# Kernel tuning notes

Measured on AMD Instinct MI355X. Metric: run time of the kernel, lower is better.

The kernel has to match this reference:

```python
import jax, jax.numpy as jnp
import numpy as np

BETA = 0.25
N_E = 1024
E_DIM = 64
B, L = 32, 2048


def setup_inputs() -> dict:
    key = jax.random.key(0)
    k1, k2 = jax.random.split(key)
    z = jax.random.normal(k1, (B, L, E_DIM), dtype=jnp.float32)
    # torch init: uniform_(-1/n_e, 1/n_e)
    codebook = jax.random.uniform(k2, (N_E, E_DIM), dtype=jnp.float32,
                                  minval=-1.0 / N_E, maxval=1.0 / N_E)
    return {"z": z, "codebook": codebook}


def reference(z, codebook):
    sg = jax.lax.stop_gradient
    n_e = codebook.shape[0]
    zf = z.reshape(-1, codebook.shape[1])  # (N, e_dim)
    # squared-distance matrix: ||z||^2 + ||e||^2 - 2 z.e  -> (N, n_e)
    d = (jnp.sum(zf * zf, axis=1, keepdims=True)
         + jnp.sum(codebook * codebook, axis=1)
         - 2.0 * zf @ codebook.T)
    idx = jnp.argmin(d, axis=1)  # (N,)
    # one-hot @ codebook is just a gather
    z_q = codebook[idx].reshape(z.shape)
    loss = (jnp.mean((sg(z_q) - z) ** 2)
            + BETA * jnp.mean((z_q - sg(z)) ** 2))
    # straight-through estimator
    z_q_st = z + sg(z_q - z)
    # codebook usage stats (mean of one-hot rows == normalized histogram)
    counts = jnp.zeros((n_e,), dtype=z.dtype).at[idx].add(1.0)
    e_mean = counts / idx.shape[0]
    perplexity = jnp.exp(-jnp.sum(e_mean * jnp.log(e_mean + 1e-10)))
    return loss, z_q_st, perplexity, idx
```

## Files before the change

### kernel.cpp

```cpp
#include <hip/hip_runtime.h>
#include <math.h>

#define E_DIM 64
#define N_E   1024
#define BETA  0.25
#define NROWS 65536

using bf16x8 = __attribute__((ext_vector_type(8))) short;
using f32x4  = __attribute__((ext_vector_type(4))) float;
#define MFMA(a, b, c) __builtin_amdgcn_mfma_f32_16x16x32_bf16((a), (b), (c), 0, 0, 0)


__device__ __forceinline__ unsigned short f2bf_rn(float f) {
    unsigned u = __builtin_bit_cast(unsigned, f);
    unsigned r = u + 0x7fffu + ((u >> 16) & 1u);
    return (unsigned short)(r >> 16);
}
__device__ __forceinline__ float bf2f(unsigned short b) {
    unsigned u = ((unsigned)b) << 16;
    return __builtin_bit_cast(float, u);
}

__device__ __forceinline__ float pw64_sq(const float* v) {
    float r[8];
#pragma unroll
    for (int l = 0; l < 8; ++l) r[l] = v[l] * v[l];
#pragma unroll
    for (int t = 1; t < 8; ++t)
#pragma unroll
        for (int l = 0; l < 8; ++l) r[l] += v[8 * t + l] * v[8 * t + l];
    return ((r[0] + r[1]) + (r[2] + r[3])) + ((r[4] + r[5]) + (r[6] + r[7]));
}

__global__ __launch_bounds__(256) void k_prep(const float* __restrict__ cb,
                                              unsigned short* __restrict__ ebh,
                                              unsigned short* __restrict__ ebl,
                                              float* __restrict__ h,
                                              unsigned* __restrict__ hist,
                                              double* __restrict__ sse,
                                              unsigned* __restrict__ flagN) {
    int t = blockIdx.x * 256 + threadIdx.x;
    {
        int e = t & 7, lane = (t >> 3) & 63, ks = (t >> 9) & 1, ct = t >> 10;
        int j = ct * 16 + (lane & 15);
        int k = ks * 32 + ((lane >> 4) << 3) + e;
        float v = cb[j * 64 + k];
        unsigned short hi = f2bf_rn(v);
        ebh[t] = hi;
        ebl[t] = f2bf_rn(v - bf2f(hi));
    }
    if (blockIdx.x < 4) {
        int j = t;
        float e[E_DIM];
        const float4* ep = reinterpret_cast<const float4*>(cb + (size_t)j * E_DIM);
#pragma unroll
        for (int k4 = 0; k4 < E_DIM / 4; ++k4) {
            float4 v = ep[k4];
            e[4 * k4 + 0] = v.x; e[4 * k4 + 1] = v.y;
            e[4 * k4 + 2] = v.z; e[4 * k4 + 3] = v.w;
        }
        h[j] = pw64_sq(e);
    } else if (blockIdx.x == 4) {
#pragma unroll
        for (int u = 0; u < 4; ++u) hist[threadIdx.x * 4 + u] = 0u;
    } else if (blockIdx.x == 5 && threadIdx.x == 0) {
        *sse = 0.0;
        *flagN = 0u;
    }
}

__global__ __launch_bounds__(512, 4) void k_mfma(
    const float* __restrict__ z, const float* __restrict__ cb,
    const float* __restrict__ h,
    const unsigned short* __restrict__ ebh, const unsigned short* __restrict__ ebl,
    float* __restrict__ out_zq, float* __restrict__ out_idx,
    unsigned* __restrict__ hist, double* __restrict__ sse,
    unsigned* __restrict__ flagN, unsigned* __restrict__ flagL) {
    const int lane = threadIdx.x & 63;
    const int w = __builtin_amdgcn_readfirstlane(threadIdx.x >> 6);
    const int m = lane & 15, g = lane >> 4;
    const int half = w >> 2;
    const int rw   = w & 3;

    __shared__ int bok;
    __shared__ float sh_h[N_E];
    __shared__ float rsv[128];
    __shared__ float sb0[2][128], sb1[2][128];
    __shared__ int   sbi[2][128];
    __shared__ float wp[8];
    if (threadIdx.x == 0) bok = 1;
    for (int i = threadIdx.x; i < N_E; i += 512) sh_h[i] = h[i];
    __syncthreads();

    {
        bf16x8 a, b;
#pragma unroll
        for (int e = 0; e < 8; ++e) {
            int k = g * 8 + e;
            a[e] = (short)f2bf_rn((float)(((m * 3 + k * 7) & 15) - 7));
            b[e] = (short)f2bf_rn((float)(((k * 5 + m * 3) & 15) - 8));
        }
        f32x4 acc = {0.f, 0.f, 0.f, 0.f};
        acc = MFMA(a, b, acc);
        bool ok = true;
#pragma unroll
        for (int r = 0; r < 4; ++r) {
            int rr = g * 4 + r;
            float E = 0.f;
            for (int k = 0; k < 32; ++k)
                E += (float)((((rr * 3 + k * 7) & 15) - 7) * (((k * 5 + m * 3) & 15) - 8));
            ok = ok && (acc[r] == E);
        }
        if (!ok) atomicAnd(&bok, 0);
    }
    __syncthreads();
    if (!bok) {
        if (threadIdx.x < 128) {
            unsigned p = atomicAdd(flagN, 1u);
            flagL[p] = (unsigned)(blockIdx.x * 128 + threadIdx.x);
        }
        return;
    }

    const int rowb32 = blockIdx.x * 128 + rw * 32;
    bf16x8 a0h0, a0l0, a0h1, a0l1, a1h0, a1l0, a1h1, a1l1;
#define ALOAD(P, AH0, AL0, AH1, AL1) {                                         \
        const int rowA = rowb32 + (P) * 16 + m;                                \
        const float4* zr = reinterpret_cast<const float4*>(z + (size_t)rowA * 64); \
        float4 p0 = zr[g * 2], p1 = zr[g * 2 + 1];                             \
        float4 p2 = zr[8 + g * 2], p3 = zr[9 + g * 2];                         \
        float t0[8] = {p0.x, p0.y, p0.z, p0.w, p1.x, p1.y, p1.z, p1.w};        \
        float t1[8] = {p2.x, p2.y, p2.z, p2.w, p3.x, p3.y, p3.z, p3.w};        \
        float s = 0.f;                                                         \
        _Pragma("unroll")                                                      \
        for (int e = 0; e < 8; ++e) {                                          \
            s += fabsf(t0[e]) + fabsf(t1[e]);                                  \
            float x0 = 2.0f * t0[e]; unsigned short h0 = f2bf_rn(x0);          \
            AH0[e] = (short)h0; AL0[e] = (short)f2bf_rn(x0 - bf2f(h0));        \
            float x1 = 2.0f * t1[e]; unsigned short h1 = f2bf_rn(x1);          \
            AH1[e] = (short)h1; AL1[e] = (short)f2bf_rn(x1 - bf2f(h1));        \
        }                                                                      \
        s += __shfl_xor(s, 16);                                                \
        s += __shfl_xor(s, 32);                                                \
        if (g == 0 && half == 0) rsv[rw * 32 + (P) * 16 + m] = s;              \
    }
    ALOAD(0, a0h0, a0l0, a0h1, a0l1)
    ALOAD(1, a1h0, a1l0, a1h1, a1l1)
#undef ALOAD

    float bb00 = INFINITY, bb01 = INFINITY, bb02 = INFINITY, bb03 = INFINITY;
    float bb10 = INFINITY, bb11 = INFINITY, bb12 = INFINITY, bb13 = INFINITY;
    float ss00 = INFINITY, ss01 = INFINITY, ss02 = INFINITY, ss03 = INFINITY;
    float ss10 = INFINITY, ss11 = INFINITY, ss12 = INFINITY, ss13 = INFINITY;
    int   ii00 = 0, ii01 = 0, ii02 = 0, ii03 = 0;
    int   ii10 = 0, ii11 = 0, ii12 = 0, ii13 = 0;
#define UPD(S, B0, B1, I0) { float _s = (S);                                   \
        if (_s < B0) { B1 = B0; B0 = _s; I0 = j; } else B1 = fminf(B1, _s); }

    const bf16x8* pBh = reinterpret_cast<const bf16x8*>(ebh);
    const bf16x8* pBl = reinterpret_cast<const bf16x8*>(ebl);
    const int ct0 = half * 32;

    bf16x8 Ah0 = pBh[ct0 * 128 + lane],        Ah1 = pBh[ct0 * 128 + lane + 64];
    bf16x8 Al0 = pBl[ct0 * 128 + lane],        Al1 = pBl[ct0 * 128 + lane + 64];
    bf16x8 Bh0 = pBh[(ct0 + 1) * 128 + lane],  Bh1 = pBh[(ct0 + 1) * 128 + lane + 64];
    bf16x8 Bl0 = pBl[(ct0 + 1) * 128 + lane],  Bl1 = pBl[(ct0 + 1) * 128 + lane + 64];

#define COLTILE(CT, VH0, VH1, VL0, VL1) {                                      \
        const int j = (CT) * 16 + m;                                           \
        const float hj = sh_h[j];                                              \
        const f32x4 z4 = {0.f, 0.f, 0.f, 0.f};                                 \
        f32x4 s0 = MFMA(a0h0, VH0, z4);                                        \
        f32x4 s1 = MFMA(a1h0, VH0, z4);                                        \
        s0 = MFMA(a0h1, VH1, s0);                                              \
        s1 = MFMA(a1h1, VH1, s1);                                              \
        s0 = MFMA(a0h0, VL0, s0);                                              \
        s1 = MFMA(a1h0, VL0, s1);                                              \
        s0 = MFMA(a0h1, VL1, s0);                                              \
        s1 = MFMA(a1h1, VL1, s1);                                              \
        s0 = MFMA(a0l0, VH0, s0);                                              \
        s1 = MFMA(a1l0, VH0, s1);                                              \
        s0 = MFMA(a0l1, VH1, s0);                                              \
        s1 = MFMA(a1l1, VH1, s1);                                              \
        UPD(hj - s0[0], bb00, ss00, ii00)                                      \
        UPD(hj - s0[1], bb01, ss01, ii01)                                      \
        UPD(hj - s0[2], bb02, ss02, ii02)                                      \
        UPD(hj - s0[3], bb03, ss03, ii03)                                      \
        UPD(hj - s1[0], bb10, ss10, ii10)                                      \
        UPD(hj - s1[1], bb11, ss11, ii11)                                      \
        UPD(hj - s1[2], bb12, ss12, ii12)                                      \
        UPD(hj - s1[3], bb13, ss13, ii13)                                      \
    }

#pragma unroll 1
    for (int ct = ct0; ct < ct0 + 32; ct += 2) {
        COLTILE(ct, Ah0, Ah1, Al0, Al1);
        if (ct + 2 < ct0 + 32) {
            const int fb = (ct + 2) * 128 + lane;
            Ah0 = pBh[fb]; Ah1 = pBh[fb + 64];
            Al0 = pBl[fb]; Al1 = pBl[fb + 64];
        }
        COLTILE(ct + 1, Bh0, Bh1, Bl0, Bl1);
        if (ct + 3 < ct0 + 32) {
            const int fb = (ct + 3) * 128 + lane;
            Bh0 = pBh[fb]; Bh1 = pBh[fb + 64];
            Bl0 = pBl[fb]; Bl1 = pBl[fb + 64];
        }
    }
#undef COLTILE
#undef UPD

#pragma unroll
    for (int mask = 1; mask < 16; mask <<= 1) {
#define MRG(B0, I0, B1) { float ob0 = __shfl_xor(B0, mask); int oi = __shfl_xor(I0, mask); \
        float ob1 = __shfl_xor(B1, mask); \
        if (ob0 < B0) { B1 = fminf(fminf(B0, B1), ob1); B0 = ob0; I0 = oi; } \
        else { B1 = fminf(B1, fminf(ob0, ob1)); } }
        MRG(bb00, ii00, ss00) MRG(bb01, ii01, ss01)
        MRG(bb02, ii02, ss02) MRG(bb03, ii03, ss03)
        MRG(bb10, ii10, ss10) MRG(bb11, ii11, ss11)
        MRG(bb12, ii12, ss12) MRG(bb13, ii13, ss13)
#undef MRG
    }

    if (m == 0) {
        const int r0 = rw * 32 + g * 4;
        sb0[half][r0 + 0] = bb00; sb1[half][r0 + 0] = ss00; sbi[half][r0 + 0] = ii00;
        sb0[half][r0 + 1] = bb01; sb1[half][r0 + 1] = ss01; sbi[half][r0 + 1] = ii01;
        sb0[half][r0 + 2] = bb02; sb1[half][r0 + 2] = ss02; sbi[half][r0 + 2] = ii02;
        sb0[half][r0 + 3] = bb03; sb1[half][r0 + 3] = ss03; sbi[half][r0 + 3] = ii03;
        const int r1 = r0 + 16;
        sb0[half][r1 + 0] = bb10; sb1[half][r1 + 0] = ss10; sbi[half][r1 + 0] = ii10;
        sb0[half][r1 + 1] = bb11; sb1[half][r1 + 1] = ss11; sbi[half][r1 + 1] = ii11;
        sb0[half][r1 + 2] = bb12; sb1[half][r1 + 2] = ss12; sbi[half][r1 + 2] = ii12;
        sb0[half][r1 + 3] = bb13; sb1[half][r1 + 3] = ss13; sbi[half][r1 + 3] = ii13;
    }
    __syncthreads();

    {
        const int rloc = threadIdx.x >> 2, q = threadIdx.x & 3;
        const int rowO = blockIdx.x * 128 + rloc;
        float b0 = sb0[0][rloc], b1 = sb1[0][rloc];
        int   vi = sbi[0][rloc];
        {
            float c0 = sb0[1][rloc], c1 = sb1[1][rloc];
            int   ci = sbi[1][rloc];
            if (c0 < b0) { b1 = fminf(b0, c1); b0 = c0; vi = ci; }
            else         { b1 = fminf(b1, c0); }
        }
        const float Delta = 6e-8f * rsv[rloc] + 2.2e-5f;
        float local = 0.f;
        if (b1 - b0 <= Delta) {
            if (q == 0) { unsigned p = atomicAdd(flagN, 1u); flagL[p] = (unsigned)rowO; }
        } else {
            if (q == 0) { out_idx[rowO] = (float)vi; atomicAdd(&hist[vi], 1u); }
            const float4* cv = reinterpret_cast<const float4*>(cb + (size_t)vi * 64) + q * 4;
            const float4* zv = reinterpret_cast<const float4*>(z + (size_t)rowO * 64) + q * 4;
            float* orow = out_zq + (size_t)rowO * 64 + q * 16;
#pragma unroll
            for (int u = 0; u < 4; ++u) {
                float4 cc = cv[u], zo = zv[u];
                orow[4 * u + 0] = cc.x; orow[4 * u + 1] = cc.y;
                orow[4 * u + 2] = cc.z; orow[4 * u + 3] = cc.w;
                float dx = cc.x - zo.x, dy = cc.y - zo.y;
                float dz = cc.z - zo.z, dw = cc.w - zo.w;
                local = fmaf(dx, dx, local); local = fmaf(dy, dy, local);
                local = fmaf(dz, dz, local); local = fmaf(dw, dw, local);
            }
        }
#pragma unroll
        for (int off = 32; off; off >>= 1) local += __shfl_down(local, off);
        if (lane == 0) wp[w] = local;
    }
    __syncthreads();
    if (threadIdx.x == 0) {
        float t = ((wp[0] + wp[1]) + (wp[2] + wp[3]))
                + ((wp[4] + wp[5]) + (wp[6] + wp[7]));
        atomicAdd(sse, (double)t);
    }
}

__global__ __launch_bounds__(64, 4) void k_cleanup(
    const float* __restrict__ z, const float* __restrict__ cb,
    const float* __restrict__ h,
    const unsigned* __restrict__ flagN, const unsigned* __restrict__ flagL,
    float* __restrict__ out_zq, float* __restrict__ out_idx,
    unsigned* __restrict__ hist, double* __restrict__ sse) {
    const unsigned n = *flagN;
    const int lane = threadIdx.x;

    for (unsigned f = blockIdx.x; f < n; f += gridDim.x) {
        const int row = (int)flagL[f];

        float tz[E_DIM];
        const float4* zp = reinterpret_cast<const float4*>(z + (size_t)row * 64);
#pragma unroll
        for (int k4 = 0; k4 < 16; ++k4) {
            float4 v = zp[k4];
            tz[4 * k4 + 0] = v.x; tz[4 * k4 + 1] = v.y;
            tz[4 * k4 + 2] = v.z; tz[4 * k4 + 3] = v.w;
        }
        const float nz = pw64_sq(tz);
#pragma unroll
        for (int k = 0; k < 64; ++k) tz[k] = 2.0f * tz[k];

        float bs = INFINITY;
        int bj = 0;
#pragma unroll 2
        for (int t = 0; t < 16; ++t) {
            const int j = lane + 64 * t;
            const float4* cv = reinterpret_cast<const float4*>(cb + (size_t)j * 64);
            float mm = 0.f;
#pragma unroll
            for (int k4 = 0; k4 < 16; ++k4) {
                float4 e = cv[k4];
                mm = fmaf(tz[4 * k4 + 0], e.x, mm);
                mm = fmaf(tz[4 * k4 + 1], e.y, mm);
                mm = fmaf(tz[4 * k4 + 2], e.z, mm);
                mm = fmaf(tz[4 * k4 + 3], e.w, mm);
            }
            float sc = (nz + h[j]) - mm;
            if (sc < bs) { bs = sc; bj = j; }
        }
#pragma unroll
        for (int off = 32; off; off >>= 1) {
            float s2 = __shfl_down(bs, off);
            int   j2 = __shfl_down(bj, off);
            if (s2 < bs || (s2 == bs && j2 < bj)) { bs = s2; bj = j2; }
        }
        bj = __shfl(bj, 0);

        float c = cb[(size_t)bj * 64 + lane];
        out_zq[(size_t)row * 64 + lane] = c;
        float d = c - 0.5f * tz[lane];
        float l2 = d * d;
#pragma unroll
        for (int off = 32; off; off >>= 1) l2 += __shfl_down(l2, off);
        if (lane == 0) {
            out_idx[row] = (float)bj;
            atomicAdd(&hist[bj], 1u);
            atomicAdd(sse, (double)l2);
        }
    }
}

__global__ __launch_bounds__(256) void k_h_fb(const float* __restrict__ cb,
                                              float* __restrict__ h) {
    int j = blockIdx.x * 256 + threadIdx.x;
    if (j < N_E) {
        float e[E_DIM];
        const float4* ep = reinterpret_cast<const float4*>(cb + (size_t)j * E_DIM);
#pragma unroll
        for (int k4 = 0; k4 < E_DIM / 4; ++k4) {
            float4 v = ep[k4];
            e[4 * k4 + 0] = v.x; e[4 * k4 + 1] = v.y;
            e[4 * k4 + 2] = v.z; e[4 * k4 + 3] = v.w;
        }
        h[j] = pw64_sq(e);
    }
}

__global__ __launch_bounds__(512, 2) void k_scan_fb(
    const float* __restrict__ z, const float* __restrict__ cb,
    const float* __restrict__ h,
    float* __restrict__ out_zq, float* __restrict__ out_idx,
    unsigned* __restrict__ hist, double* __restrict__ sse) {
    const int lane = threadIdx.x & 63;
    const int w = __builtin_amdgcn_readfirstlane(threadIdx.x >> 6);
    const int row = blockIdx.x * 64 + lane;
    float tz[E_DIM];
    const float4* zp = reinterpret_cast<const float4*>(z + (size_t)row * E_DIM);
#pragma unroll
    for (int k4 = 0; k4 < E_DIM / 4; ++k4) {
        float4 v = zp[k4];
        tz[4 * k4 + 0] = v.x; tz[4 * k4 + 1] = v.y;
        tz[4 * k4 + 2] = v.z; tz[4 * k4 + 3] = v.w;
    }
    const float nz = pw64_sq(tz);
#pragma unroll
    for (int k = 0; k < E_DIM; ++k) tz[k] = 2.0f * tz[k];
    float b0 = INFINITY; int bi = 0;
    const int j0 = w * 128;
#pragma unroll 1
    for (int j = j0; j < j0 + 128; j += 4) {
        const float* c0 = cb + (size_t)j * E_DIM;
        float m0 = 0.f, m1 = 0.f, m2 = 0.f, m3 = 0.f;
#pragma unroll
        for (int k = 0; k < E_DIM; ++k) {
            float wk = tz[k];
            m0 = fmaf(wk, c0[0 * E_DIM + k], m0);
            m1 = fmaf(wk, c0[1 * E_DIM + k], m1);
            m2 = fmaf(wk, c0[2 * E_DIM + k], m2);
            m3 = fmaf(wk, c0[3 * E_DIM + k], m3);
        }
        float s0 = (nz + h[j + 0]) - m0;
        float s1 = (nz + h[j + 1]) - m1;
        float s2 = (nz + h[j + 2]) - m2;
        float s3 = (nz + h[j + 3]) - m3;
        if (s0 < b0) { b0 = s0; bi = j + 0; }
        if (s1 < b0) { b0 = s1; bi = j + 1; }
        if (s2 < b0) { b0 = s2; bi = j + 2; }
        if (s3 < b0) { b0 = s3; bi = j + 3; }
    }
    __shared__ float lb[8][64];
    __shared__ int   li[8][64];
    lb[w][lane] = b0; li[w][lane] = bi;
    __syncthreads();
    if (threadIdx.x < 64) {
        float b = lb[0][lane]; int i = li[0][lane];
#pragma unroll
        for (int c = 1; c < 8; ++c) {
            float bc = lb[c][lane]; int ic = li[c][lane];
            if (bc < b) { b = bc; i = ic; }
        }
        out_idx[row] = (float)i;
        float local = 0.f;
        const float4* cv = reinterpret_cast<const float4*>(cb + (size_t)i * E_DIM);
        float* orow = out_zq + (size_t)row * E_DIM;
#pragma unroll
        for (int k4 = 0; k4 < E_DIM / 4; ++k4) {
            float4 c = cv[k4];
            float zx = 0.5f * tz[4 * k4 + 0], zy = 0.5f * tz[4 * k4 + 1];
            float zz = 0.5f * tz[4 * k4 + 2], zw = 0.5f * tz[4 * k4 + 3];
            orow[4 * k4 + 0] = c.x; orow[4 * k4 + 1] = c.y;
            orow[4 * k4 + 2] = c.z; orow[4 * k4 + 3] = c.w;
            float dx = c.x - zx, dy = c.y - zy, dz = c.z - zz, dw = c.w - zw;
            local = fmaf(dx, dx, local); local = fmaf(dy, dy, local);
            local = fmaf(dz, dz, local); local = fmaf(dw, dw, local);
        }
        atomicAdd(&hist[i], 1u);
#pragma unroll
        for (int off = 32; off; off >>= 1) local += __shfl_down(local, off);
        if (lane == 0) atomicAdd(sse, (double)local);
    }
}

__global__ __launch_bounds__(256) void k_final(
    const unsigned* __restrict__ hist, const double* __restrict__ sse,
    float* __restrict__ out, int nrows) {
    __shared__ double sh[256];
    double acc = 0.0;
    for (int j = threadIdx.x; j < N_E; j += 256) {
        double p = (double)hist[j] / (double)nrows;
        acc += p * log(p + 1e-10);
    }
    sh[threadIdx.x] = acc;
    __syncthreads();
    for (int s = 128; s; s >>= 1) {
        if (threadIdx.x < s) sh[threadIdx.x] += sh[threadIdx.x + s];
        __syncthreads();
    }
    if (threadIdx.x == 0) {
        double ntot = (double)nrows * (double)E_DIM;
        out[0] = (float)((1.0 + BETA) * (*sse) / ntot);
        out[1 + (size_t)nrows * E_DIM] = (float)exp(-sh[0]);
    }
}

extern "C" void kernel_launch(void* const* d_in, const int* in_sizes, int n_in,
                              void* d_out, int out_size, void* d_ws, size_t ws_size,
                              hipStream_t stream) {
    const float* z  = (const float*)d_in[0];
    const float* cb = (const float*)d_in[1];
    const int nrows = in_sizes[0] / E_DIM;
    float* out = (float*)d_out;

    char* ws = (char*)d_ws;
    unsigned* hist  = (unsigned*)(ws + 0);
    double*   sse   = (double*)  (ws + 4096);
    unsigned* flagN = (unsigned*)(ws + 4104);
    float*    h     = (float*)   (ws + 4112);
    unsigned short* ebh = (unsigned short*)(ws + 8208);
    unsigned short* ebl = (unsigned short*)(ws + 139280);
    unsigned* flagL = (unsigned*)(ws + 270352);

    float* out_zq  = out + 1;
    float* out_idx = out + 1 + (size_t)nrows * E_DIM + 1;

    if (ws_size >= 532496) {
        k_prep<<<256, 256, 0, stream>>>(cb, ebh, ebl, h, hist, sse, flagN);
        k_mfma<<<nrows / 128, 512, 0, stream>>>(z, cb, h, ebh, ebl,
                                                out_zq, out_idx, hist, sse,
                                                flagN, flagL);
        k_cleanup<<<2048, 64, 0, stream>>>(z, cb, h, flagN, flagL,
                                           out_zq, out_idx, hist, sse);
    } else {
        hipMemsetAsync(d_ws, 0, 4112, stream);
        k_h_fb<<<(N_E + 255) / 256, 256, 0, stream>>>(cb, h);
        k_scan_fb<<<nrows / 64, 512, 0, stream>>>(z, cb, h, out_zq, out_idx, hist, sse);
    }
    k_final<<<1, 256, 0, stream>>>(hist, sse, out, nrows);
}
```

Baseline: 102.2 us.

## Split codebook four ways per block and halve rows per block

Each block now handles 64 rows instead of 128, with its 8 waves arranged as 2 row groups by 4 codebook quarters rather than 4 row groups by 2 halves. The grid doubles to 1024 blocks, and each wave's MFMA loop over codebook tiles is half as long. The cross-wave merge now combines four partial top-2 results per row. The aim is more blocks and shorter serial per-wave loops, for better load balance and latency hiding. In exchange, each codebook tile is loaded by more blocks and per-block fixed costs grow, including the MFMA self-test and loading the h table into LDS.

```diff
diff --git a/kernel.cpp b/kernel.cpp
--- a/kernel.cpp
+++ b/kernel.cpp
@@ -79,14 +79,14 @@
     const int lane = threadIdx.x & 63;
     const int w = __builtin_amdgcn_readfirstlane(threadIdx.x >> 6);
     const int m = lane & 15, g = lane >> 4;
-    const int half = w >> 2;
-    const int rw   = w & 3;
+    const int q4 = w >> 1;
+    const int rw = w & 1;
 
     __shared__ int bok;
     __shared__ float sh_h[N_E];
-    __shared__ float rsv[128];
-    __shared__ float sb0[2][128], sb1[2][128];
-    __shared__ int   sbi[2][128];
+    __shared__ float rsv[64];
+    __shared__ float sb0[4][64], sb1[4][64];
+    __shared__ int   sbi[4][64];
     __shared__ float wp[8];
     if (threadIdx.x == 0) bok = 1;
     for (int i = threadIdx.x; i < N_E; i += 512) sh_h[i] = h[i];
@@ -115,14 +115,14 @@
     }
     __syncthreads();
     if (!bok) {
-        if (threadIdx.x < 128) {
+        if (threadIdx.x < 64) {
             unsigned p = atomicAdd(flagN, 1u);
-            flagL[p] = (unsigned)(blockIdx.x * 128 + threadIdx.x);
+            flagL[p] = (unsigned)(blockIdx.x * 64 + threadIdx.x);
         }
         return;
     }
 
-    const int rowb32 = blockIdx.x * 128 + rw * 32;
+    const int rowb32 = blockIdx.x * 64 + rw * 32;
     bf16x8 a0h0, a0l0, a0h1, a0l1, a1h0, a1l0, a1h1, a1l1;
 #define ALOAD(P, AH0, AL0, AH1, AL1) {                                         \
         const int rowA = rowb32 + (P) * 16 + m;                                \
@@ -142,7 +142,7 @@
         }                                                                      \
         s += __shfl_xor(s, 16);                                                \
         s += __shfl_xor(s, 32);                                                \
-        if (g == 0 && half == 0) rsv[rw * 32 + (P) * 16 + m] = s;              \
+        if (g == 0 && q4 == 0) rsv[rw * 32 + (P) * 16 + m] = s;                \
     }
     ALOAD(0, a0h0, a0l0, a0h1, a0l1)
     ALOAD(1, a1h0, a1l0, a1h1, a1l1)
@@ -159,7 +159,7 @@
 
     const bf16x8* pBh = reinterpret_cast<const bf16x8*>(ebh);
     const bf16x8* pBl = reinterpret_cast<const bf16x8*>(ebl);
-    const int ct0 = half * 32;
+    const int ct0 = q4 * 16;
 
     bf16x8 Ah0 = pBh[ct0 * 128 + lane],        Ah1 = pBh[ct0 * 128 + lane + 64];
     bf16x8 Al0 = pBl[ct0 * 128 + lane],        Al1 = pBl[ct0 * 128 + lane + 64];
@@ -193,15 +193,15 @@
     }
 
 #pragma unroll 1
-    for (int ct = ct0; ct < ct0 + 32; ct += 2) {
+    for (int ct = ct0; ct < ct0 + 16; ct += 2) {
         COLTILE(ct, Ah0, Ah1, Al0, Al1);
-        if (ct + 2 < ct0 + 32) {
+        if (ct + 2 < ct0 + 16) {
             const int fb = (ct + 2) * 128 + lane;
             Ah0 = pBh[fb]; Ah1 = pBh[fb + 64];
             Al0 = pBl[fb]; Al1 = pBl[fb + 64];
         }
         COLTILE(ct + 1, Bh0, Bh1, Bl0, Bl1);
-        if (ct + 3 < ct0 + 32) {
+        if (ct + 3 < ct0 + 16) {
             const int fb = (ct + 3) * 128 + lane;
             Bh0 = pBh[fb]; Bh1 = pBh[fb + 64];
             Bl0 = pBl[fb]; Bl1 = pBl[fb + 64];
@@ -225,28 +225,29 @@
 
     if (m == 0) {
         const int r0 = rw * 32 + g * 4;
-        sb0[half][r0 + 0] = bb00; sb1[half][r0 + 0] = ss00; sbi[half][r0 + 0] = ii00;
-        sb0[half][r0 + 1] = bb01; sb1[half][r0 + 1] = ss01; sbi[half][r0 + 1] = ii01;
-        sb0[half][r0 + 2] = bb02; sb1[half][r0 + 2] = ss02; sbi[half][r0 + 2] = ii02;
-        sb0[half][r0 + 3] = bb03; sb1[half][r0 + 3] = ss03; sbi[half][r0 + 3] = ii03;
+        sb0[q4][r0 + 0] = bb00; sb1[q4][r0 + 0] = ss00; sbi[q4][r0 + 0] = ii00;
+        sb0[q4][r0 + 1] = bb01; sb1[q4][r0 + 1] = ss01; sbi[q4][r0 + 1] = ii01;
+        sb0[q4][r0 + 2] = bb02; sb1[q4][r0 + 2] = ss02; sbi[q4][r0 + 2] = ii02;
+        sb0[q4][r0 + 3] = bb03; sb1[q4][r0 + 3] = ss03; sbi[q4][r0 + 3] = ii03;
         const int r1 = r0 + 16;
-        sb0[half][r1 + 0] = bb10; sb1[half][r1 + 0] = ss10; sbi[half][r1 + 0] = ii10;
-        sb0[half][r1 + 1] = bb11; sb1[half][r1 + 1] = ss11; sbi[half][r1 + 1] = ii11;
-        sb0[half][r1 + 2] = bb12; sb1[half][r1 + 2] = ss12; sbi[half][r1 + 2] = ii12;
-        sb0[half][r1 + 3] = bb13; sb1[half][r1 + 3] = ss13; sbi[half][r1 + 3] = ii13;
+        sb0[q4][r1 + 0] = bb10; sb1[q4][r1 + 0] = ss10; sbi[q4][r1 + 0] = ii10;
+        sb0[q4][r1 + 1] = bb11; sb1[q4][r1 + 1] = ss11; sbi[q4][r1 + 1] = ii11;
+        sb0[q4][r1 + 2] = bb12; sb1[q4][r1 + 2] = ss12; sbi[q4][r1 + 2] = ii12;
+        sb0[q4][r1 + 3] = bb13; sb1[q4][r1 + 3] = ss13; sbi[q4][r1 + 3] = ii13;
     }
     __syncthreads();
 
     {
-        const int rloc = threadIdx.x >> 2, q = threadIdx.x & 3;
-        const int rowO = blockIdx.x * 128 + rloc;
+        const int rloc = threadIdx.x >> 3, q = threadIdx.x & 7;
+        const int rowO = blockIdx.x * 64 + rloc;
         float b0 = sb0[0][rloc], b1 = sb1[0][rloc];
         int   vi = sbi[0][rloc];
-        {
-            float c0 = sb0[1][rloc], c1 = sb1[1][rloc];
-            int   ci = sbi[1][rloc];
+#pragma unroll
+        for (int c = 1; c < 4; ++c) {
+            float c0 = sb0[c][rloc], c1 = sb1[c][rloc];
+            int   ci = sbi[c][rloc];
             if (c0 < b0) { b1 = fminf(b0, c1); b0 = c0; vi = ci; }
-            else         { b1 = fminf(b1, c0); }
+            else         { b1 = fminf(b1, fminf(c0, c1)); }
         }
         const float Delta = 6e-8f * rsv[rloc] + 2.2e-5f;
         float local = 0.f;
@@ -254,11 +255,11 @@
             if (q == 0) { unsigned p = atomicAdd(flagN, 1u); flagL[p] = (unsigned)rowO; }
         } else {
             if (q == 0) { out_idx[rowO] = (float)vi; atomicAdd(&hist[vi], 1u); }
-            const float4* cv = reinterpret_cast<const float4*>(cb + (size_t)vi * 64) + q * 4;
-            const float4* zv = reinterpret_cast<const float4*>(z + (size_t)rowO * 64) + q * 4;
-            float* orow = out_zq + (size_t)rowO * 64 + q * 16;
-#pragma unroll
-            for (int u = 0; u < 4; ++u) {
+            const float4* cv = reinterpret_cast<const float4*>(cb + (size_t)vi * 64) + q * 2;
+            const float4* zv = reinterpret_cast<const float4*>(z + (size_t)rowO * 64) + q * 2;
+            float* orow = out_zq + (size_t)rowO * 64 + q * 8;
+#pragma unroll
+            for (int u = 0; u < 2; ++u) {
                 float4 cc = cv[u], zo = zv[u];
                 orow[4 * u + 0] = cc.x; orow[4 * u + 1] = cc.y;
                 orow[4 * u + 2] = cc.z; orow[4 * u + 3] = cc.w;
@@ -479,9 +480,9 @@
 
     if (ws_size >= 532496) {
         k_prep<<<256, 256, 0, stream>>>(cb, ebh, ebl, h, hist, sse, flagN);
-        k_mfma<<<nrows / 128, 512, 0, stream>>>(z, cb, h, ebh, ebl,
-                                                out_zq, out_idx, hist, sse,
-                                                flagN, flagL);
+        k_mfma<<<nrows / 64, 512, 0, stream>>>(z, cb, h, ebh, ebl,
+                                               out_zq, out_idx, hist, sse,
+                                               flagN, flagL);
         k_cleanup<<<2048, 64, 0, stream>>>(z, cb, h, flagN, flagL,
                                            out_zq, out_idx, hist, sse);
     } else {
```

Result: slower. 115.0 us (+12.5%).
